# Kernel optimization log

Measured on AMD Instinct MI355X. Metric: run time of the kernel, lower is better.

The kernel has to match this reference:

```python
import jax, jax.numpy as jnp
import numpy as np

D_X = D_Z = D_ATTN = D_OUT = 2048
L_Z = 32768


def setup_inputs() -> dict:
    key = jax.random.key(0)
    ks = jax.random.split(key, 8)
    xavier_q = (2.0 / (D_X + D_ATTN)) ** 0.5
    xavier_k = (2.0 / (D_Z + D_ATTN)) ** 0.5
    xavier_v = (2.0 / (D_Z + D_OUT)) ** 0.5
    return {
        "x": jax.random.normal(ks[0], (D_X,), jnp.float32),
        "zs": jax.random.normal(ks[1], (L_Z, D_Z), jnp.float32),
        "x_mask": 1,
        "zs_mask": jax.random.randint(ks[2], (L_Z,), 0, 2, jnp.int64.dtype if jax.config.read('jax_enable_x64') else jnp.int32),
        "w_q": jax.random.normal(ks[3], (D_X, D_ATTN), jnp.float32) * xavier_q,
        "w_k": jax.random.normal(ks[4], (D_Z, D_ATTN), jnp.float32) * xavier_k,
        "w_v": jax.random.normal(ks[5], (D_Z, D_OUT), jnp.float32) * xavier_v,
        "b_q": jnp.zeros((D_ATTN,), jnp.float32),
        "b_k": jnp.zeros((D_ATTN,), jnp.float32),
        "b_v": jnp.zeros((D_OUT,), jnp.float32),
    }


def reference(x, zs, x_mask, zs_mask, w_q, w_k, w_v, b_q, b_k, b_v):
    scale = 1.0 / jnp.sqrt(jnp.asarray(w_q.shape[1], x.dtype))
    q = x @ w_q + b_q                       # [d_attn]
    k = zs @ w_k + b_k                      # [l_z, d_attn]
    v = zs @ w_v + b_v                      # [l_z, d_out]
    score = (k @ q) * scale                 # [l_z]
    mask = (x_mask * zs_mask).astype(score.dtype)  # [l_z]
    bmask = mask != 0
    neg = jnp.finfo(score.dtype).min
    masked_score = jnp.where(bmask, score, neg)
    attention = jax.nn.softmax(masked_score, axis=-1) * mask  # [l_z]
    vt = attention @ v                      # [d_out] (vectorized form of the python loop)
    return (q, k, v, score, mask, masked_score, attention, vt)
```

## Files before the change

kernel.cpp:

```cpp
#include <hip/hip_runtime.h>
#include <hip/hip_bf16.h>
#include <cfloat>

#define DD   2048
#define LZ   32768
#define SCALE_Q 0.022097086912079608f

#define NEG_SENTINEL (-3.3895313892515355e38f)

typedef __bf16          bf16x8   __attribute__((ext_vector_type(8)));
typedef float           f32x4    __attribute__((ext_vector_type(4)));
typedef unsigned short  ushort8v __attribute__((ext_vector_type(8)));
typedef unsigned short  ushort4v __attribute__((ext_vector_type(4)));
typedef unsigned short  ushort_t;

typedef __attribute__((address_space(1))) const unsigned int guint_t;
typedef __attribute__((address_space(3))) unsigned int       luint_t;

__device__ __forceinline__ void gload16(const void* g, void* l) {
    __builtin_amdgcn_global_load_lds((guint_t*)g, (luint_t*)l, 16, 0, 0);
}

__device__ __forceinline__ unsigned short bf16_rne(float x) {
    unsigned u = __builtin_bit_cast(unsigned, x);
    u += 0x7fffu + ((u >> 16) & 1u);
    return (unsigned short)(u >> 16);
}

__device__ __forceinline__ void split_bf16(float x, unsigned short& hi, unsigned short& lo) {
    unsigned u = __builtin_bit_cast(unsigned, x);
    hi = (unsigned short)(u >> 16);
    float r = x - __builtin_bit_cast(float, u & 0xffff0000u);
    unsigned v = __builtin_bit_cast(unsigned, r);
    v += 0x7fffu + ((v >> 16) & 1u);
    lo = (unsigned short)(v >> 16);
}

#define TILE_US 8192

__global__ __launch_bounds__(256) void init_qvt(const float* __restrict__ b_q,
                                                float* __restrict__ q,
                                                float* __restrict__ vt) {
    int i = blockIdx.x * 256 + threadIdx.x;
    q[i]  = b_q[i];
    vt[i] = 0.0f;
}

__global__ __launch_bounds__(256) void q_gemv(const float* __restrict__ x,
                                              const float* __restrict__ w_q,
                                              float* __restrict__ q) {
    int n  = blockIdx.x * 256 + threadIdx.x;
    int c0 = blockIdx.y * 128;
    float acc = 0.0f;
    for (int c = 0; c < 128; ++c)
        acc = fmaf(x[c0 + c], w_q[(size_t)(c0 + c) * DD + n], acc);
    atomicAdd(&q[n], acc);
}

__global__ __launch_bounds__(256) void prea_kernel(const float* __restrict__ zs,
                                                   ushort_t* __restrict__ a_ws) {
    const int T = blockIdx.x;
    const int p = blockIdx.y;
    const int t = threadIdx.x;
    ushort_t* tile = a_ws + ((size_t)p * 32 + T) * TILE_US;
    #pragma unroll
    for (int j = 0; j < 4; ++j) {
        const int idx = t + j * 256;
        const int row = idx >> 3, k8 = idx & 7;
        const float4* src = (const float4*)(zs + ((size_t)p * 128 + row) * DD + T * 64 + k8 * 8);
        float4 f0 = src[0], f1 = src[1];
        ushort8v hv;
        hv[0] = bf16_rne(f0.x); hv[1] = bf16_rne(f0.y);
        hv[2] = bf16_rne(f0.z); hv[3] = bf16_rne(f0.w);
        hv[4] = bf16_rne(f1.x); hv[5] = bf16_rne(f1.y);
        hv[6] = bf16_rne(f1.z); hv[7] = bf16_rne(f1.w);
        const int phys = k8 ^ (row & 7);
        *(ushort8v*)(tile + (row * 8 + phys) * 8) = hv;
    }
}

__global__ __launch_bounds__(256) void preb_kernel(const float* __restrict__ w_k,
                                                   const float* __restrict__ w_v,
                                                   ushort_t* __restrict__ b_ws) {
    __shared__ float tile[64][65];
    const int mat = blockIdx.z;
    const float* w = mat ? w_v : w_k;
    const int T = blockIdx.x;
    const int kt0 = T * 64, nt0 = blockIdx.y * 64;
    const int t = threadIdx.x;
    const int rl  = t >> 4;
    const int cl4 = (t & 15) * 4;
    #pragma unroll
    for (int j = 0; j < 4; ++j) {
        float4 v4 = *(const float4*)&w[(size_t)(kt0 + rl + j * 16) * DD + nt0 + cl4];
        tile[rl + j * 16][cl4 + 0] = v4.x;
        tile[rl + j * 16][cl4 + 1] = v4.y;
        tile[rl + j * 16][cl4 + 2] = v4.z;
        tile[rl + j * 16][cl4 + 3] = v4.w;
    }
    __syncthreads();
    #pragma unroll
    for (int jj = 0; jj < 2; ++jj) {
        const int idx = t + jj * 256;
        const int n_l = idx >> 3, k8 = idx & 7;
        const int ng    = mat * DD + nt0 + n_l;
        const int panel = ng >> 7, prow = ng & 127;
        ushort8v hv;
        #pragma unroll
        for (int e = 0; e < 8; ++e)
            hv[e] = bf16_rne(tile[k8 * 8 + e][n_l]);
        ushort_t* dst = b_ws + ((size_t)panel * 32 + T) * TILE_US;
        const int phys = k8 ^ (prow & 7);
        *(ushort8v*)(dst + (prow * 8 + phys) * 8) = hv;
    }
}

__device__ __forceinline__ void vm_wait8() { asm volatile("s_waitcnt vmcnt(8)" ::: "memory"); }
__device__ __forceinline__ void vm_wait0() { asm volatile("s_waitcnt vmcnt(0)" ::: "memory"); }

__device__ __forceinline__ void kv_stage(const ushort_t* __restrict__ a_blk,
                                         const ushort_t* __restrict__ b_blk,
                                         char* LdsA, char* LdsB,
                                         int T, int wid, int lane) {
    const int p = T & 1;
    const bool isA = wid < 4;
    const int w4 = isA ? wid : wid - 4;
    const int h = w4 >> 1, qr = w4 & 1;
    const ushort_t* src = (isA ? a_blk : b_blk) + ((size_t)h * 32 + T) * TILE_US + qr * 4096;
    char* dst = (isA ? LdsA : LdsB) + p * 32768 + h * 16384 + qr * 8192;
    #pragma unroll
    for (int i = 0; i < 8; ++i) {
        const int g = i * 64 + lane;
        gload16(src + (size_t)g * 8, dst + g * 16);
    }
}

#define CLUSTER(AF, BF, R0)                                                              \
    {                                                                                    \
        _Pragma("unroll")                                                                \
        for (int i2 = 0; i2 < 4; ++i2) {                                                 \
            _Pragma("unroll")                                                            \
            for (int j = 0; j < 4; ++j)                                                  \
                acc[(R0) + i2][j] = __builtin_amdgcn_mfma_f32_16x16x32_bf16(             \
                    AF[i2], BF[j], acc[(R0) + i2][j], 0, 0, 0);                          \
        }                                                                                \
    }

#define LD8(dst, base, off)                                                              \
    dst = __builtin_bit_cast(bf16x8, *(const ushort8v*)((base) + (off)));

#define LGKM(N)  asm volatile("s_waitcnt lgkmcnt(" #N ")" ::: "memory")

template<int TAIL>
__device__ __forceinline__ void kv_iter(
    const ushort_t* __restrict__ a_blk, const ushort_t* __restrict__ b_blk,
    char* LdsA, char* LdsB, int T,
    int wid, int lane, int wm, int wn,
    int soh, int sol, int arow, int brow,
    bf16x8 (&a0)[4], bf16x8 (&b0)[4],
    f32x4 (&acc)[8][4])
{
    const int p = T & 1;
    const char* Ab = LdsA + p * 32768 + wm * 16384;
    const char* Bb = LdsB + p * 32768 + (wn >> 1) * 16384;

    bf16x8 a1[4], a2[4], a3[4], b1[4];

    #pragma unroll
    for (int i = 0; i < 4; ++i) LD8(a1[i], Ab, arow + (4 + i) * 2048 + soh);
    #pragma unroll
    for (int i = 0; i < 4; ++i) LD8(a2[i], Ab, arow + i * 2048 + sol);
    LGKM(8);
    __builtin_amdgcn_sched_barrier(0);
    __builtin_amdgcn_s_setprio(1);
    CLUSTER(a0, b0, 0);
    __builtin_amdgcn_s_setprio(0);

    #pragma unroll
    for (int i = 0; i < 4; ++i) LD8(a3[i], Ab, arow + (4 + i) * 2048 + sol);
    #pragma unroll
    for (int j = 0; j < 4; ++j) LD8(b1[j], Bb, brow + j * 2048 + sol);
    LGKM(8);
    __builtin_amdgcn_sched_barrier(0);
    __builtin_amdgcn_s_setprio(1);
    CLUSTER(a1, b0, 4);
    __builtin_amdgcn_s_setprio(0);

    LGKM(0);
    __builtin_amdgcn_sched_barrier(0);
    __builtin_amdgcn_s_barrier();

    if (TAIL == 0) kv_stage(a_blk, b_blk, LdsA, LdsB, T + 2, wid, lane);
    __builtin_amdgcn_sched_barrier(0);
    __builtin_amdgcn_s_setprio(1);
    CLUSTER(a2, b1, 0);
    __builtin_amdgcn_s_setprio(0);

    if (TAIL == 0) vm_wait8();
    if (TAIL == 1) vm_wait0();
    __builtin_amdgcn_sched_barrier(0);
    __builtin_amdgcn_s_barrier();

    if (TAIL <= 1) {
        const int np = (T + 1) & 1;
        const char* Abn = LdsA + np * 32768 + wm * 16384;
        const char* Bbn = LdsB + np * 32768 + (wn >> 1) * 16384;
        #pragma unroll
        for (int i = 0; i < 4; ++i) LD8(a0[i], Abn, arow + i * 2048 + soh);
        #pragma unroll
        for (int j = 0; j < 4; ++j) LD8(b0[j], Bbn, brow + j * 2048 + soh);
    }
    __builtin_amdgcn_sched_barrier(0);
    __builtin_amdgcn_s_setprio(1);
    CLUSTER(a3, b1, 4);
    __builtin_amdgcn_s_setprio(0);
}

__global__ __launch_bounds__(512, 2)
void kv_gemm256(const ushort_t* __restrict__ a_ws, const ushort_t* __restrict__ b_ws,
                const float* __restrict__ b_k, const float* __restrict__ b_v,
                const float* __restrict__ qvec, float* __restrict__ rawpart,
                float* __restrict__ out_k, float* __restrict__ out_v)
{
    __shared__ char LdsA[2 * 32768];
    __shared__ char LdsB[2 * 32768];

    const int tid  = threadIdx.x;
    const int wid  = tid >> 6;
    const int lane = tid & 63;
    const int wm   = wid >> 2;
    const int wn   = wid & 3;
    const int lrow = lane & 15;
    const int lq   = lane >> 4;

    const int lin = blockIdx.x;
    const int swz = (lin & 7) * 256 + (lin >> 3);
    const int nb  = swz & 15;
    const int mb  = swz >> 4;

    const int m0   = mb * 256;
    const int n0   = nb * 256;
    const int mat  = n0 >> 11;
    const int nloc = n0 & (DD - 1);

    const ushort_t* a_blk = a_ws + (size_t)(mb * 2) * 32 * TILE_US;
    const ushort_t* b_blk = b_ws + (size_t)(nb * 2) * 32 * TILE_US;

    const int soh  = ((lq       ^ (lrow & 7)) << 4);
    const int sol  = (((lq | 4) ^ (lrow & 7)) << 4);
    const int arow = lrow * 128;
    const int brow = (wn & 1) * 8192 + lrow * 128;

    f32x4 acc[8][4] = {};
    bf16x8 a0[4], b0[4];

    kv_stage(a_blk, b_blk, LdsA, LdsB, 0, wid, lane);
    kv_stage(a_blk, b_blk, LdsA, LdsB, 1, wid, lane);
    vm_wait8();
    __builtin_amdgcn_sched_barrier(0);
    __builtin_amdgcn_s_barrier();
    {
        const char* Ab0 = LdsA + wm * 16384;
        const char* Bb0 = LdsB + (wn >> 1) * 16384;
        #pragma unroll
        for (int i = 0; i < 4; ++i) LD8(a0[i], Ab0, arow + i * 2048 + soh);
        #pragma unroll
        for (int j = 0; j < 4; ++j) LD8(b0[j], Bb0, brow + j * 2048 + soh);
    }

    for (int T = 0; T < 30; ++T)
        kv_iter<0>(a_blk, b_blk, LdsA, LdsB, T, wid, lane, wm, wn,
                   soh, sol, arow, brow, a0, b0, acc);
    kv_iter<1>(a_blk, b_blk, LdsA, LdsB, 30, wid, lane, wm, wn,
               soh, sol, arow, brow, a0, b0, acc);
    kv_iter<2>(a_blk, b_blk, LdsA, LdsB, 31, wid, lane, wm, wn,
               soh, sol, arow, brow, a0, b0, acc);

    const float* bias = mat ? b_v : b_k;
    float* outp = mat ? out_v : out_k;
    const int lq4 = lq * 4;
    float bv[4], qv[4];
    #pragma unroll
    for (int j = 0; j < 4; ++j) {
        const int nout = nloc + wn * 64 + j * 16 + lrow;
        bv[j] = bias[nout];
        qv[j] = qvec[nout];
    }
    #pragma unroll
    for (int j = 0; j < 4; ++j) {
        const int nout = nloc + wn * 64 + j * 16 + lrow;
        #pragma unroll
        for (int i = 0; i < 8; ++i) {
            const int mbase = m0 + wm * 128 + i * 16 + lq4;
            #pragma unroll
            for (int r = 0; r < 4; ++r)
                outp[(size_t)(mbase + r) * DD + nout] = acc[i][j][r] + bv[j];
        }
    }
    if (mat == 0) {
        float* rp = rawpart + (size_t)nb * LZ;
        #pragma unroll
        for (int i = 0; i < 8; ++i) {
            #pragma unroll
            for (int r = 0; r < 4; ++r) {
                float psum = 0.0f;
                #pragma unroll
                for (int j = 0; j < 4; ++j)
                    psum = fmaf(acc[i][j][r] + bv[j], qv[j], psum);
                psum += __shfl_xor(psum, 1);
                psum += __shfl_xor(psum, 2);
                psum += __shfl_xor(psum, 4);
                psum += __shfl_xor(psum, 8);
                if (lrow == 0)
                    rp[m0 + wm * 128 + i * 16 + lq4 + r] = psum;
            }
        }
    }
}

__global__ __launch_bounds__(256)
void kv_gemm_fb(const float* __restrict__ zs,
                const float* __restrict__ w_k, const float* __restrict__ w_v,
                const float* __restrict__ b_k, const float* __restrict__ b_v,
                float* __restrict__ out_k, float* __restrict__ out_v)
{
    __shared__ ushort_t As[128 * 64];
    __shared__ ushort_t Bs[128 * 64];

    const int tid  = threadIdx.x;
    const int m0   = blockIdx.y * 128;
    const int n0   = blockIdx.x * 128;
    const int mat  = n0 >> 11;
    const int nloc = n0 & (DD - 1);

    const int wid  = tid >> 6;
    const int lane = tid & 63;
    const int wm   = wid >> 1;
    const int wn   = wid & 1;
    const int lrow = lane & 15;
    const int lq   = lane >> 4;

    int aoff_hi[4], aoff_lo[4], boff_hi[4], boff_lo[4];
    #pragma unroll
    for (int i = 0; i < 4; ++i) {
        const int ra = wm * 64 + i * 16 + lrow;
        aoff_hi[i] = ra * 128 + ((lq       ^ (ra & 7)) * 16);
        aoff_lo[i] = ra * 128 + (((lq + 4) ^ (ra & 7)) * 16);
        const int rb = wn * 64 + i * 16 + lrow;
        boff_hi[i] = rb * 128 + ((lq       ^ (rb & 7)) * 16);
        boff_lo[i] = rb * 128 + (((lq + 4) ^ (rb & 7)) * 16);
    }

    f32x4 acc[4][4] = {};
    const int srow  = tid >> 1;
    const int shalf = tid & 1;

    for (int ks = 0; ks < 64; ++ks) {
        {
            const float4* ap = (const float4*)(zs + (size_t)(m0 + srow) * DD + ks * 32 + shalf * 16);
            float4 f0 = ap[0], f1 = ap[1], f2 = ap[2], f3 = ap[3];
            float e[16] = {f0.x,f0.y,f0.z,f0.w, f1.x,f1.y,f1.z,f1.w,
                           f2.x,f2.y,f2.z,f2.w, f3.x,f3.y,f3.z,f3.w};
            ushort8v h0, h1, l0, l1;
            #pragma unroll
            for (int c = 0; c < 8; ++c) {
                unsigned short hh, ll;
                split_bf16(e[c], hh, ll);
                h0[c] = hh; l0[c] = ll;
                split_bf16(e[8 + c], hh, ll);
                h1[c] = hh; l1[c] = ll;
            }
            char* rowbase = (char*)As + srow * 128;
            const int s0 = (shalf * 2)     ^ (srow & 7);
            const int s1 = (shalf * 2 + 1) ^ (srow & 7);
            *(ushort8v*)(rowbase + s0 * 16)       = h0;
            *(ushort8v*)(rowbase + s1 * 16)       = h1;
            *(ushort8v*)(rowbase + (s0 ^ 4) * 16) = l0;
            *(ushort8v*)(rowbase + (s1 ^ 4) * 16) = l1;
        }
        {
            const float* w = mat ? w_v : w_k;
            const int k_l = (tid >> 5) * 4;
            const int n_l = (tid & 31) * 4;
            float4 r0 = *(const float4*)&w[(size_t)(ks * 32 + k_l + 0) * DD + nloc + n_l];
            float4 r1 = *(const float4*)&w[(size_t)(ks * 32 + k_l + 1) * DD + nloc + n_l];
            float4 r2 = *(const float4*)&w[(size_t)(ks * 32 + k_l + 2) * DD + nloc + n_l];
            float4 r3 = *(const float4*)&w[(size_t)(ks * 32 + k_l + 3) * DD + nloc + n_l];
            float el[4][4] = {{r0.x,r0.y,r0.z,r0.w},{r1.x,r1.y,r1.z,r1.w},
                              {r2.x,r2.y,r2.z,r2.w},{r3.x,r3.y,r3.z,r3.w}};
            const int slot = k_l >> 3, sub = ((k_l >> 2) & 1) * 8;
            #pragma unroll
            for (int c = 0; c < 4; ++c) {
                const int n = n_l + c;
                ushort4v hv, lv;
                #pragma unroll
                for (int r = 0; r < 4; ++r) {
                    unsigned short hh, ll;
                    split_bf16(el[r][c], hh, ll);
                    hv[r] = hh; lv[r] = ll;
                }
                char* rb = (char*)Bs + n * 128;
                const int sp = slot ^ (n & 7);
                *(ushort4v*)(rb + sp * 16 + sub)       = hv;
                *(ushort4v*)(rb + (sp ^ 4) * 16 + sub) = lv;
            }
        }
        __syncthreads();

        bf16x8 a_hi[4], a_lo[4], b_hi[4], b_lo[4];
        #pragma unroll
        for (int i = 0; i < 4; ++i) {
            a_hi[i] = __builtin_bit_cast(bf16x8, *(const ushort8v*)((const char*)As + aoff_hi[i]));
            a_lo[i] = __builtin_bit_cast(bf16x8, *(const ushort8v*)((const char*)As + aoff_lo[i]));
            b_hi[i] = __builtin_bit_cast(bf16x8, *(const ushort8v*)((const char*)Bs + boff_hi[i]));
            b_lo[i] = __builtin_bit_cast(bf16x8, *(const ushort8v*)((const char*)Bs + boff_lo[i]));
        }
        #pragma unroll
        for (int i = 0; i < 4; ++i)
            #pragma unroll
            for (int j = 0; j < 4; ++j)
                acc[i][j] = __builtin_amdgcn_mfma_f32_16x16x32_bf16(a_hi[i], b_hi[j], acc[i][j], 0, 0, 0);
        #pragma unroll
        for (int i = 0; i < 4; ++i)
            #pragma unroll
            for (int j = 0; j < 4; ++j)
                acc[i][j] = __builtin_amdgcn_mfma_f32_16x16x32_bf16(a_hi[i], b_lo[j], acc[i][j], 0, 0, 0);
        #pragma unroll
        for (int i = 0; i < 4; ++i)
            #pragma unroll
            for (int j = 0; j < 4; ++j)
                acc[i][j] = __builtin_amdgcn_mfma_f32_16x16x32_bf16(a_lo[i], b_hi[j], acc[i][j], 0, 0, 0);
        __syncthreads();
    }

    const float* bias = mat ? b_v : b_k;
    float* outp = mat ? out_v : out_k;
    #pragma unroll
    for (int j = 0; j < 4; ++j) {
        const int nout = nloc + wn * 64 + j * 16 + lrow;
        const float bv = bias[nout];
        #pragma unroll
        for (int i = 0; i < 4; ++i) {
            const int mbase = m0 + wm * 64 + i * 16 + lq * 4;
            #pragma unroll
            for (int r = 0; r < 4; ++r)
                outp[(size_t)(mbase + r) * DD + nout] = acc[i][j][r] + bv;
        }
    }
}

__global__ __launch_bounds__(256) void score_raw_kernel(const float* __restrict__ k,
                                                        const float* __restrict__ q,
                                                        float* __restrict__ raw) {
    const int wid = threadIdx.x >> 6, lane = threadIdx.x & 63;
    const int l = blockIdx.x * 4 + wid;
    const float4* krow = (const float4*)(k + (size_t)l * DD);
    const float4* q4   = (const float4*)q;
    float acc = 0.0f;
    #pragma unroll
    for (int it = 0; it < 8; ++it) {
        float4 kv = krow[lane + it * 64];
        float4 qv = q4[lane + it * 64];
        acc = fmaf(kv.x, qv.x, acc);
        acc = fmaf(kv.y, qv.y, acc);
        acc = fmaf(kv.z, qv.z, acc);
        acc = fmaf(kv.w, qv.w, acc);
    }
    #pragma unroll
    for (int off = 32; off; off >>= 1) acc += __shfl_xor(acc, off, 64);
    if (lane == 0) raw[l] = acc;
}

__global__ __launch_bounds__(256) void finalize_score(const float* parts,
                                                      int nparts,
                                                      const int* __restrict__ x_mask,
                                                      const int* __restrict__ zs_mask,
                                                      float* __restrict__ score,
                                                      float* __restrict__ maskv,
                                                      float* masked) {
    const int i = blockIdx.x * 256 + threadIdx.x;
    float rawv = 0.0f;
    for (int p = 0; p < nparts; ++p)
        rawv += parts[(size_t)p * LZ + i];
    const float s = rawv * SCALE_Q;
    const float m = (float)(x_mask[0] * zs_mask[i]);
    score[i]  = s;
    maskv[i]  = m;
    masked[i] = (m != 0.0f) ? s : NEG_SENTINEL;
}

__global__ __launch_bounds__(1024) void softmax_kernel(const float* __restrict__ masked,
                                                       const float* __restrict__ maskv,
                                                       float* __restrict__ attention) {
    __shared__ float red[16];
    __shared__ float gsh[2];
    const int t = threadIdx.x;
    const int wid = t >> 6, lane = t & 63;

    float msv[32];
    float mx = -FLT_MAX;
    #pragma unroll
    for (int c = 0; c < 32; ++c) {
        msv[c] = masked[t + c * 1024];
        mx = fmaxf(mx, msv[c]);
    }
    #pragma unroll
    for (int off = 32; off; off >>= 1) mx = fmaxf(mx, __shfl_xor(mx, off, 64));
    if (lane == 0) red[wid] = mx;
    __syncthreads();
    if (t == 0) {
        float g = red[0];
        for (int i = 1; i < 16; ++i) g = fmaxf(g, red[i]);
        gsh[0] = g;
    }
    __syncthreads();
    const float gmax = gsh[0];

    float s = 0.0f;
    #pragma unroll
    for (int c = 0; c < 32; ++c) {
        const float e = expf(msv[c] - gmax);
        msv[c] = e;
        s += e;
    }
    #pragma unroll
    for (int off = 32; off; off >>= 1) s += __shfl_xor(s, off, 64);
    if (lane == 0) red[wid] = s;
    __syncthreads();
    if (t == 0) {
        float g = 0.0f;
        for (int i = 0; i < 16; ++i) g += red[i];
        gsh[1] = g;
    }
    __syncthreads();
    const float inv = 1.0f / gsh[1];

    #pragma unroll
    for (int c = 0; c < 32; ++c) {
        const int i = t + c * 1024;
        attention[i] = msv[c] * inv * maskv[i];
    }
}

__global__ __launch_bounds__(256) void vt_kernel(const float* __restrict__ v,
                                                 const float* __restrict__ attention,
                                                 float* __restrict__ vt) {
    __shared__ float att_s[512];
    const int t = threadIdx.x;
    const int d = blockIdx.x * 256 + t;
    const int l0 = blockIdx.y * 512;
    att_s[t]       = attention[l0 + t];
    att_s[t + 256] = attention[l0 + t + 256];
    __syncthreads();
    float acc = 0.0f;
    const float* vp = v + (size_t)l0 * DD + d;
    for (int i = 0; i < 512; ++i)
        acc = fmaf(att_s[i], vp[(size_t)i * DD], acc);
    atomicAdd(&vt[d], acc);
}

extern "C" void kernel_launch(void* const* d_in, const int* in_sizes, int n_in,
                              void* d_out, int out_size, void* d_ws, size_t ws_size,
                              hipStream_t stream) {
    const float* x       = (const float*)d_in[0];
    const float* zs      = (const float*)d_in[1];
    const int*   x_mask  = (const int*)d_in[2];
    const int*   zs_mask = (const int*)d_in[3];
    const float* w_q     = (const float*)d_in[4];
    const float* w_k     = (const float*)d_in[5];
    const float* w_v     = (const float*)d_in[6];
    const float* b_q     = (const float*)d_in[7];
    const float* b_k     = (const float*)d_in[8];
    const float* b_v     = (const float*)d_in[9];

    float* out       = (float*)d_out;
    float* q         = out;
    float* k         = q + DD;
    float* v         = k + (size_t)LZ * DD;
    float* score     = v + (size_t)LZ * DD;
    float* maskv     = score + LZ;
    float* masked    = maskv + LZ;
    float* attention = masked + LZ;
    float* vt        = attention + LZ;

    init_qvt<<<8, 256, 0, stream>>>(b_q, q, vt);
    q_gemv<<<dim3(8, 16), 256, 0, stream>>>(x, w_q, q);

    const size_t A_WS = (size_t)256 * 32 * TILE_US * sizeof(ushort_t);
    const size_t B_WS = (size_t)32  * 32 * TILE_US * sizeof(ushort_t);
    const size_t R_WS = (size_t)8 * LZ * sizeof(float);

    if (ws_size >= A_WS + B_WS + R_WS) {
        ushort_t* a_ws = (ushort_t*)d_ws;
        ushort_t* b_ws = (ushort_t*)((char*)d_ws + A_WS);
        float* rawpart = (float*)((char*)d_ws + A_WS + B_WS);
        prea_kernel<<<dim3(32, 256), 256, 0, stream>>>(zs, a_ws);
        preb_kernel<<<dim3(32, 32, 2), 256, 0, stream>>>(w_k, w_v, b_ws);
        kv_gemm256<<<2048, 512, 0, stream>>>(a_ws, b_ws, b_k, b_v, q, rawpart, k, v);
        finalize_score<<<128, 256, 0, stream>>>(rawpart, 8, x_mask, zs_mask,
                                                score, maskv, masked);
    } else {
        kv_gemm_fb<<<dim3(32, 256), 256, 0, stream>>>(zs, w_k, w_v, b_k, b_v, k, v);
        score_raw_kernel<<<8192, 256, 0, stream>>>(k, q, masked);
        finalize_score<<<128, 256, 0, stream>>>(masked, 1, x_mask, zs_mask,
                                                score, maskv, masked);
    }

    softmax_kernel<<<1, 1024, 0, stream>>>(masked, maskv, attention);
    vt_kernel<<<dim3(8, 64), 256, 0, stream>>>(v, attention, vt);
}
```

Baseline: 747.1 us.

## Split GEMM block work across 16 waves with 64x64 per-wave tiles

The 256x256 KV GEMM block goes from 8 waves (each computing 128x64) to 16 waves of 1024 threads (each computing 64x64). The hand-interleaved register prefetch pipeline is replaced by a simpler load-all-then-compute loop, and the global-to-LDS staging is spread over all 16 waves. Score partials are now written per wave column, so finalize reads 32 partials instead of 8. This trades fewer accumulators and registers per wave for less LDS/MFMA overlap within each wave, and relies on more waves to hide latency. It may also reduce occupancy to one block per CU.

```diff
diff --git a/kernel.cpp b/kernel.cpp
--- a/kernel.cpp
+++ b/kernel.cpp
@@ -115,108 +115,90 @@
     }
 }
 
-__device__ __forceinline__ void vm_wait8() { asm volatile("s_waitcnt vmcnt(8)" ::: "memory"); }
+__device__ __forceinline__ void vm_wait4() { asm volatile("s_waitcnt vmcnt(4)" ::: "memory"); }
 __device__ __forceinline__ void vm_wait0() { asm volatile("s_waitcnt vmcnt(0)" ::: "memory"); }
 
-__device__ __forceinline__ void kv_stage(const ushort_t* __restrict__ a_blk,
-                                         const ushort_t* __restrict__ b_blk,
-                                         char* LdsA, char* LdsB,
-                                         int T, int wid, int lane) {
+__device__ __forceinline__ void kv_stage16(const ushort_t* __restrict__ a_blk,
+                                           const ushort_t* __restrict__ b_blk,
+                                           char* LdsA, char* LdsB,
+                                           int T, int wid, int lane) {
     const int p = T & 1;
-    const bool isA = wid < 4;
-    const int w4 = isA ? wid : wid - 4;
-    const int h = w4 >> 1, qr = w4 & 1;
-    const ushort_t* src = (isA ? a_blk : b_blk) + ((size_t)h * 32 + T) * TILE_US + qr * 4096;
-    char* dst = (isA ? LdsA : LdsB) + p * 32768 + h * 16384 + qr * 8192;
-    #pragma unroll
-    for (int i = 0; i < 8; ++i) {
+    const bool isA = wid < 8;
+    const int sw = wid & 7;
+    const int h = sw >> 2, q = sw & 3;
+    const ushort_t* src = (isA ? a_blk : b_blk) + ((size_t)h * 32 + T) * TILE_US + q * 2048;
+    char* dst = (isA ? LdsA : LdsB) + p * 32768 + h * 16384 + q * 4096;
+    #pragma unroll
+    for (int i = 0; i < 4; ++i) {
         const int g = i * 64 + lane;
         gload16(src + (size_t)g * 8, dst + g * 16);
     }
 }
 
-#define CLUSTER(AF, BF, R0)                                                              \
+#define CLUSTER16(AF, BF)                                                                \
     {                                                                                    \
         _Pragma("unroll")                                                                \
         for (int i2 = 0; i2 < 4; ++i2) {                                                 \
             _Pragma("unroll")                                                            \
-            for (int j = 0; j < 4; ++j)                                                  \
-                acc[(R0) + i2][j] = __builtin_amdgcn_mfma_f32_16x16x32_bf16(             \
-                    AF[i2], BF[j], acc[(R0) + i2][j], 0, 0, 0);                          \
+            for (int j2 = 0; j2 < 4; ++j2)                                               \
+                acc[i2][j2] = __builtin_amdgcn_mfma_f32_16x16x32_bf16(                   \
+                    AF[i2], BF[j2], acc[i2][j2], 0, 0, 0);                               \
         }                                                                                \
     }
 
 #define LD8(dst, base, off)                                                              \
     dst = __builtin_bit_cast(bf16x8, *(const ushort8v*)((base) + (off)));
 
-#define LGKM(N)  asm volatile("s_waitcnt lgkmcnt(" #N ")" ::: "memory")
+#define LGKM0()  asm volatile("s_waitcnt lgkmcnt(0)" ::: "memory")
 
 template<int TAIL>
-__device__ __forceinline__ void kv_iter(
+__device__ __forceinline__ void kv_iter16(
     const ushort_t* __restrict__ a_blk, const ushort_t* __restrict__ b_blk,
     char* LdsA, char* LdsB, int T,
     int wid, int lane, int wm, int wn,
-    int soh, int sol, int arow, int brow,
-    bf16x8 (&a0)[4], bf16x8 (&b0)[4],
-    f32x4 (&acc)[8][4])
+    int soh, int sol, int arow,
+    f32x4 (&acc)[4][4])
 {
     const int p = T & 1;
-    const char* Ab = LdsA + p * 32768 + wm * 16384;
-    const char* Bb = LdsB + p * 32768 + (wn >> 1) * 16384;
-
-    bf16x8 a1[4], a2[4], a3[4], b1[4];
-
-    #pragma unroll
-    for (int i = 0; i < 4; ++i) LD8(a1[i], Ab, arow + (4 + i) * 2048 + soh);
-    #pragma unroll
-    for (int i = 0; i < 4; ++i) LD8(a2[i], Ab, arow + i * 2048 + sol);
-    LGKM(8);
+    const char* Ab = LdsA + p * 32768 + (wm >> 1) * 16384 + (wm & 1) * 8192;
+    const char* Bb = LdsB + p * 32768 + (wn >> 1) * 16384 + (wn & 1) * 8192;
+
+    bf16x8 a[4], b[4];
+
+    #pragma unroll
+    for (int i = 0; i < 4; ++i) LD8(a[i], Ab, arow + i * 2048 + soh);
+    #pragma unroll
+    for (int j = 0; j < 4; ++j) LD8(b[j], Bb, arow + j * 2048 + soh);
+    LGKM0();
     __builtin_amdgcn_sched_barrier(0);
     __builtin_amdgcn_s_setprio(1);
-    CLUSTER(a0, b0, 0);
+    CLUSTER16(a, b);
     __builtin_amdgcn_s_setprio(0);
-
-    #pragma unroll
-    for (int i = 0; i < 4; ++i) LD8(a3[i], Ab, arow + (4 + i) * 2048 + sol);
-    #pragma unroll
-    for (int j = 0; j < 4; ++j) LD8(b1[j], Bb, brow + j * 2048 + sol);
-    LGKM(8);
+    __builtin_amdgcn_sched_barrier(0);
+
+    #pragma unroll
+    for (int i = 0; i < 4; ++i) LD8(a[i], Ab, arow + i * 2048 + sol);
+    #pragma unroll
+    for (int j = 0; j < 4; ++j) LD8(b[j], Bb, arow + j * 2048 + sol);
+    LGKM0();
     __builtin_amdgcn_sched_barrier(0);
     __builtin_amdgcn_s_setprio(1);
-    CLUSTER(a1, b0, 4);
+    CLUSTER16(a, b);
     __builtin_amdgcn_s_setprio(0);
-
-    LGKM(0);
     __builtin_amdgcn_sched_barrier(0);
+
+    if (TAIL == 2) return;
+
     __builtin_amdgcn_s_barrier();
 
-    if (TAIL == 0) kv_stage(a_blk, b_blk, LdsA, LdsB, T + 2, wid, lane);
-    __builtin_amdgcn_sched_barrier(0);
-    __builtin_amdgcn_s_setprio(1);
-    CLUSTER(a2, b1, 0);
-    __builtin_amdgcn_s_setprio(0);
-
-    if (TAIL == 0) vm_wait8();
+    if (TAIL == 0) kv_stage16(a_blk, b_blk, LdsA, LdsB, T + 2, wid, lane);
+    if (TAIL == 0) vm_wait4();
     if (TAIL == 1) vm_wait0();
     __builtin_amdgcn_sched_barrier(0);
     __builtin_amdgcn_s_barrier();
-
-    if (TAIL <= 1) {
-        const int np = (T + 1) & 1;
-        const char* Abn = LdsA + np * 32768 + wm * 16384;
-        const char* Bbn = LdsB + np * 32768 + (wn >> 1) * 16384;
-        #pragma unroll
-        for (int i = 0; i < 4; ++i) LD8(a0[i], Abn, arow + i * 2048 + soh);
-        #pragma unroll
-        for (int j = 0; j < 4; ++j) LD8(b0[j], Bbn, brow + j * 2048 + soh);
-    }
-    __builtin_amdgcn_sched_barrier(0);
-    __builtin_amdgcn_s_setprio(1);
-    CLUSTER(a3, b1, 4);
-    __builtin_amdgcn_s_setprio(0);
-}
-
-__global__ __launch_bounds__(512, 2)
+}
+
+__global__ __launch_bounds__(1024)
 void kv_gemm256(const ushort_t* __restrict__ a_ws, const ushort_t* __restrict__ b_ws,
                 const float* __restrict__ b_k, const float* __restrict__ b_v,
                 const float* __restrict__ qvec, float* __restrict__ rawpart,
@@ -249,32 +231,22 @@
     const int soh  = ((lq       ^ (lrow & 7)) << 4);
     const int sol  = (((lq | 4) ^ (lrow & 7)) << 4);
     const int arow = lrow * 128;
-    const int brow = (wn & 1) * 8192 + lrow * 128;
-
-    f32x4 acc[8][4] = {};
-    bf16x8 a0[4], b0[4];
-
-    kv_stage(a_blk, b_blk, LdsA, LdsB, 0, wid, lane);
-    kv_stage(a_blk, b_blk, LdsA, LdsB, 1, wid, lane);
-    vm_wait8();
+
+    f32x4 acc[4][4] = {};
+
+    kv_stage16(a_blk, b_blk, LdsA, LdsB, 0, wid, lane);
+    kv_stage16(a_blk, b_blk, LdsA, LdsB, 1, wid, lane);
+    vm_wait4();
     __builtin_amdgcn_sched_barrier(0);
     __builtin_amdgcn_s_barrier();
-    {
-        const char* Ab0 = LdsA + wm * 16384;
-        const char* Bb0 = LdsB + (wn >> 1) * 16384;
-        #pragma unroll
-        for (int i = 0; i < 4; ++i) LD8(a0[i], Ab0, arow + i * 2048 + soh);
-        #pragma unroll
-        for (int j = 0; j < 4; ++j) LD8(b0[j], Bb0, brow + j * 2048 + soh);
-    }
 
     for (int T = 0; T < 30; ++T)
-        kv_iter<0>(a_blk, b_blk, LdsA, LdsB, T, wid, lane, wm, wn,
-                   soh, sol, arow, brow, a0, b0, acc);
-    kv_iter<1>(a_blk, b_blk, LdsA, LdsB, 30, wid, lane, wm, wn,
-               soh, sol, arow, brow, a0, b0, acc);
-    kv_iter<2>(a_blk, b_blk, LdsA, LdsB, 31, wid, lane, wm, wn,
-               soh, sol, arow, brow, a0, b0, acc);
+        kv_iter16<0>(a_blk, b_blk, LdsA, LdsB, T, wid, lane, wm, wn,
+                     soh, sol, arow, acc);
+    kv_iter16<1>(a_blk, b_blk, LdsA, LdsB, 30, wid, lane, wm, wn,
+                 soh, sol, arow, acc);
+    kv_iter16<2>(a_blk, b_blk, LdsA, LdsB, 31, wid, lane, wm, wn,
+                 soh, sol, arow, acc);
 
     const float* bias = mat ? b_v : b_k;
     float* outp = mat ? out_v : out_k;
@@ -290,17 +262,17 @@
     for (int j = 0; j < 4; ++j) {
         const int nout = nloc + wn * 64 + j * 16 + lrow;
         #pragma unroll
-        for (int i = 0; i < 8; ++i) {
-            const int mbase = m0 + wm * 128 + i * 16 + lq4;
+        for (int i = 0; i < 4; ++i) {
+            const int mbase = m0 + wm * 64 + i * 16 + lq4;
             #pragma unroll
             for (int r = 0; r < 4; ++r)
                 outp[(size_t)(mbase + r) * DD + nout] = acc[i][j][r] + bv[j];
         }
     }
     if (mat == 0) {
-        float* rp = rawpart + (size_t)nb * LZ;
-        #pragma unroll
-        for (int i = 0; i < 8; ++i) {
+        float* rp = rawpart + (size_t)(nb * 4 + wn) * LZ;
+        #pragma unroll
+        for (int i = 0; i < 4; ++i) {
             #pragma unroll
             for (int r = 0; r < 4; ++r) {
                 float psum = 0.0f;
@@ -312,7 +284,7 @@
                 psum += __shfl_xor(psum, 4);
                 psum += __shfl_xor(psum, 8);
                 if (lrow == 0)
-                    rp[m0 + wm * 128 + i * 16 + lq4 + r] = psum;
+                    rp[m0 + wm * 64 + i * 16 + lq4 + r] = psum;
             }
         }
     }
@@ -588,7 +560,7 @@
 
     const size_t A_WS = (size_t)256 * 32 * TILE_US * sizeof(ushort_t);
     const size_t B_WS = (size_t)32  * 32 * TILE_US * sizeof(ushort_t);
-    const size_t R_WS = (size_t)8 * LZ * sizeof(float);
+    const size_t R_WS = (size_t)32 * LZ * sizeof(float);
 
     if (ws_size >= A_WS + B_WS + R_WS) {
         ushort_t* a_ws = (ushort_t*)d_ws;
@@ -596,8 +568,8 @@
         float* rawpart = (float*)((char*)d_ws + A_WS + B_WS);
         prea_kernel<<<dim3(32, 256), 256, 0, stream>>>(zs, a_ws);
         preb_kernel<<<dim3(32, 32, 2), 256, 0, stream>>>(w_k, w_v, b_ws);
-        kv_gemm256<<<2048, 512, 0, stream>>>(a_ws, b_ws, b_k, b_v, q, rawpart, k, v);
-        finalize_score<<<128, 256, 0, stream>>>(rawpart, 8, x_mask, zs_mask,
+        kv_gemm256<<<2048, 1024, 0, stream>>>(a_ws, b_ws, b_k, b_v, q, rawpart, k, v);
+        finalize_score<<<128, 256, 0, stream>>>(rawpart, 32, x_mask, zs_mask,
                                                 score, maskv, masked);
     } else {
         kv_gemm_fb<<<dim3(32, 256), 256, 0, stream>>>(zs, w_k, w_v, b_k, b_v, k, v);
```

Result: slower. 779.5 us (+4.3%).
